# Kernel tuning notes

Hardware: AMD Instinct MI355X
Metric: run time of the kernel (lower is better)

## Reference

```python
import jax, jax.numpy as jnp
import numpy as np

B, N, F_IN, F_OUT, H = 8, 1024, 128, 64, 4
EPS = 1e-7
NEG_SLOPE = 0.2


def setup_inputs() -> dict:
    key = jax.random.key(0)
    k_a, k_x, k_w, k_aw, k_ab = jax.random.split(key, 5)
    A = jax.random.randint(k_a, (B, N, N), 0, 2).astype(jnp.float32)
    x = jax.random.normal(k_x, (B, N, F_IN), dtype=jnp.float32)
    # per-head params (stacked over head axis): GAT.W (xavier-normal-ish), attention Linear(2F->1)
    W = jax.random.normal(k_w, (H, F_IN, F_OUT), dtype=jnp.float32) * np.sqrt(2.0 / (F_IN + F_OUT))
    lim = 1.0 / np.sqrt(2 * F_OUT)
    a_w = jax.random.uniform(k_aw, (H, 2 * F_OUT), minval=-lim, maxval=lim, dtype=jnp.float32)
    a_b = jax.random.uniform(k_ab, (H,), minval=-lim, maxval=lim, dtype=jnp.float32)
    return {"A": A, "x": x, "W": W, "a_w": a_w, "a_b": a_b}


def reference(A, x, W, a_w, a_b):
    # Wh: (B, H, N, F_OUT)
    Wh = jnp.einsum('bnf,hfo->bhno', x, W)
    # attention linear on concat([Wh_i, Wh_j]) is separable: a1.Wh_i + a2.Wh_j + b
    a1, a2 = a_w[:, :F_OUT], a_w[:, F_OUT:]
    s_i = jnp.einsum('bhno,ho->bhn', Wh, a1)   # depends on row index i (dim 1 of (B,N,N))
    s_j = jnp.einsum('bhno,ho->bhn', Wh, a2)   # depends on col index j (dim 2)
    e = s_i[:, :, :, None] + s_j[:, :, None, :] + a_b[None, :, None, None]  # (B,H,Ni,Nj)
    e = jnp.where(e >= 0, e, NEG_SLOPE * e)  # LeakyReLU(0.2)
    # masked softmax as in source: exp, mask by A, normalize over dim=1 of (B,N,N) -> axis 2 here
    exps = jnp.exp(e) * A[:, None, :, :]
    attn = exps / (jnp.sum(exps, axis=2, keepdims=True) + EPS)
    out = jnp.einsum('bhij,bhjo->bhio', attn, Wh)  # matmul over j
    # concat heads on feature dim: (B, N, H*F_OUT)
    return out.transpose(0, 2, 1, 3).reshape(B, N, H * F_OUT)
```

## Files before the change

kernel.cpp:

```cpp
#include <hip/hip_runtime.h>
#include <hip/hip_bf16.h>
#include <hip/hip_fp16.h>

#define BB 8
#define NN 1024
#define FIN 128
#define FOUT 64
#define HH 4
#define EPSV 1e-7f
#define SLOPE 0.2f
#define LOG2E 1.44269504088896340736f

typedef _Float16 v8h __attribute__((ext_vector_type(8)));
typedef _Float16 v4h __attribute__((ext_vector_type(4)));
typedef _Float16 v2h __attribute__((ext_vector_type(2)));
typedef __fp16 v2hf __attribute__((ext_vector_type(2)));
typedef float v4f __attribute__((ext_vector_type(4)));

union U8 { v2h p[4]; v8h v; };
union U2 { v2hf hf; v2h h; };

__device__ __forceinline__ v2h clamp01(v2h x) {
  v2h zero = {(_Float16)0.0f, (_Float16)0.0f};
  v2h one = {(_Float16)1.0f, (_Float16)1.0f};
  return __builtin_elementwise_min(__builtin_elementwise_max(x, zero), one);
}

__device__ __forceinline__ v2h cvt2(float a, float b) {
  U2 u;
  u.hf = __builtin_amdgcn_cvt_pkrtz(a, b);
  return u.h;
}

__device__ __forceinline__ float dot2(v2h a, v2h b, float c) {
  U2 ua, ub;
  ua.h = a;
  ub.h = b;
  return __builtin_amdgcn_fdot2(ua.hf, ub.hf, c, false);
}

__global__ __launch_bounds__(256) void k0_wt(const float* __restrict__ W,
                                             _Float16* __restrict__ Wtt) {
  for (int it = 0; it < 16; ++it) {
    int idx = blockIdx.x * 4096 + it * 256 + threadIdx.x;
    int e = idx & 7, ln = (idx >> 3) & 15, kgg = (idx >> 7) & 15,
        ct = idx >> 11;
    int c = ct * 16 + ln, k = kgg * 8 + e;
    Wtt[idx] = (_Float16)W[(size_t)(c >> 6) * 8192 + k * 64 + (c & 63)];
  }
}

__global__ __launch_bounds__(256) void k1_whm(
    const float* __restrict__ x, const _Float16* __restrict__ Wtt,
    const float* __restrict__ aw, const float* __restrict__ ab,
    _Float16* __restrict__ WhH, float* __restrict__ si2,
    float* __restrict__ tj2, _Float16* __restrict__ tjh,
    _Float16* __restrict__ djh, _Float16* __restrict__ e2jh,
    float* __restrict__ e2i_t, float* __restrict__ di_t) {
  __shared__ _Float16 xs[16][136];
  int tid = threadIdx.x;
#pragma unroll
  for (int t2 = 0; t2 < 2; ++t2) {
    int idx = t2 * 256 + tid;
    int row = idx >> 5, c4 = (idx & 31) * 4;
    float4 v = *(const float4*)(x + ((size_t)blockIdx.x * 16 + row) * FIN + c4);
    v4h hv;
    hv[0] = (_Float16)v.x; hv[1] = (_Float16)v.y;
    hv[2] = (_Float16)v.z; hv[3] = (_Float16)v.w;
    *(v4h*)(&xs[row][c4]) = hv;
  }
  __syncthreads();
  int w = tid >> 6, l = tid & 63;
  int kg = l >> 4, ln = l & 15;
  v4f acc[4] = {{}, {}, {}, {}};
#pragma unroll
  for (int ks = 0; ks < 4; ++ks) {
    v8h af = *(const v8h*)(&xs[ln][ks * 32 + kg * 8]);
    int kgg = ks * 4 + kg;
#pragma unroll
    for (int t = 0; t < 4; ++t) {
      int ct = w * 4 + t;
      v8h bf = *(const v8h*)(Wtt + (((size_t)ct * 16 + kgg) * 16 + ln) * 8);
      acc[t] = __builtin_amdgcn_mfma_f32_16x16x32_f16(af, bf, acc[t], 0, 0, 0);
    }
  }
  float a1v[4], a2v[4];
#pragma unroll
  for (int t = 0; t < 4; ++t) {
    a1v[t] = aw[w * 128 + t * 16 + ln];
    a2v[t] = aw[w * 128 + 64 + t * 16 + ln];
  }
  float abv = ab[w];
#pragma unroll
  for (int r = 0; r < 4; ++r) {
    float v1 = acc[0][r] * a1v[0] + acc[1][r] * a1v[1] +
               acc[2][r] * a1v[2] + acc[3][r] * a1v[3];
    float v2 = acc[0][r] * a2v[0] + acc[1][r] * a2v[1] +
               acc[2][r] * a2v[2] + acc[3][r] * a2v[3];
#pragma unroll
    for (int off = 1; off < 16; off <<= 1) {
      v1 += __shfl_xor(v1, off);
      v2 += __shfl_xor(v2, off);
    }
    if (ln == 0) {
      int gr = blockIdx.x * 16 + kg * 4 + r;
      int b_ = gr >> 10, n_ = gr & 1023;
      size_t row = ((size_t)b_ * HH + w) * NN + n_;
      float v1L = v1 * LOG2E;
      float tjL = (v2 + abv) * LOG2E;
      si2[row] = v1L;
      tj2[row] = tjL;
      float e1i = __builtin_amdgcn_exp2f(v1L);
      float e2i = __builtin_amdgcn_exp2f(0.2f * v1L);
      e2i_t[row] = e2i;
      di_t[row] = e1i - e2i;
      float e1j = __builtin_amdgcn_exp2f(tjL);
      float e2j = __builtin_amdgcn_exp2f(0.2f * tjL);
      tjh[row] = (_Float16)tjL;
      e2jh[row] = (_Float16)e2j;
      djh[row] = (_Float16)(e1j - e2j);
    }
  }
#pragma unroll
  for (int t = 0; t < 4; ++t) {
#pragma unroll
    for (int r = 0; r < 4; ++r) {
      int gr = blockIdx.x * 16 + kg * 4 + r;
      int b_ = gr >> 10, n_ = gr & 1023;
      WhH[(((size_t)b_ * HH + w) * NN + n_) * 64 + (t * 16 + ln)] =
          (_Float16)acc[t][r];
    }
  }
}

__global__ __launch_bounds__(256) void kb_colsum_bits(
    const float* __restrict__ A, const float* __restrict__ si2,
    const float* __restrict__ e2i_t, const float* __restrict__ di_t,
    const _Float16* __restrict__ tjh, const _Float16* __restrict__ djh,
    const _Float16* __restrict__ e2jh, float* __restrict__ part,
    unsigned long long* __restrict__ Abits) {
  __shared__ v2h si_p[4][16], di_p[4][16], e2i_p[4][16];
  int b = blockIdx.z, is = blockIdx.y, jt = blockIdx.x;
  int tid = threadIdx.x;
  int w = tid >> 6, lane = tid & 63;
  int j = jt * 256 + tid;
  int i0 = is * 32;
  if (tid < 64) {
    int h = tid >> 4, pp = tid & 15;
    size_t row = ((size_t)(b * HH + h)) * NN + i0 + 2 * pp;
    si_p[h][pp] = cvt2(si2[row], si2[row + 1]);
    di_p[h][pp] = cvt2(di_t[row], di_t[row + 1]);
    e2i_p[h][pp] = cvt2(e2i_t[row], e2i_t[row + 1]);
  }
  __syncthreads();
  v2h tjb[4], djb[4], ejb[4];
#pragma unroll
  for (int h = 0; h < 4; ++h) {
    size_t jr = ((size_t)(b * HH + h)) * NN + j;
    _Float16 t = tjh[jr], d = djh[jr], e = e2jh[jr];
    tjb[h][0] = t; tjb[h][1] = t;
    djb[h][0] = d; djb[h][1] = d;
    ejb[h][0] = e; ejb[h][1] = e;
  }
  v2h big = {(_Float16)4096.0f, (_Float16)4096.0f};
  float acc[4] = {0.f, 0.f, 0.f, 0.f};
  const float* Ap = A + ((size_t)b * NN + i0) * NN + j;
  unsigned long long myword = 0ull;
#pragma unroll
  for (int c = 0; c < 4; ++c) {
    float av[8];
#pragma unroll
    for (int q = 0; q < 8; ++q) av[q] = Ap[(size_t)(c * 8 + q) * NN];
    v2h apk[4];
#pragma unroll
    for (int q = 0; q < 4; ++q) apk[q] = cvt2(av[2 * q], av[2 * q + 1]);
#pragma unroll
    for (int q = 0; q < 8; ++q) {
      unsigned long long m = __ballot(av[q] != 0.0f);
      if (lane == c * 8 + q) myword = m;
    }
#pragma unroll
    for (int h = 0; h < 4; ++h) {
      U8 si4, di4, ei4;
      si4.v = *(const v8h*)&si_p[h][c * 4];
      di4.v = *(const v8h*)&di_p[h][c * 4];
      ei4.v = *(const v8h*)&e2i_p[h][c * 4];
#pragma unroll
      for (int pp = 0; pp < 4; ++pp) {
        v2h f = si4.p[pp] + tjb[h];
        v2h s = clamp01(f * big);
        v2h ei = s * di4.p[pp] + ei4.p[pp];
        v2h ej = s * djb[h] + ejb[h];
        v2h p = ei * ej;
        acc[h] = dot2(p, apk[pp], acc[h]);
      }
    }
  }
  if (lane < 32)
    Abits[((size_t)b * NN + i0 + lane) * 16 + jt * 4 + w] = myword;
#pragma unroll
  for (int h = 0; h < 4; ++h)
    part[((size_t)(is * 32) + b * HH + h) * NN + j] = acc[h];
}

__global__ __launch_bounds__(256) void k3_scale_tr(
    const _Float16* __restrict__ WhH, const float* __restrict__ part,
    _Float16* __restrict__ VTt) {
  __shared__ float rbuf[64];
  __shared__ _Float16 tile[64 * 66];
  int bid = blockIdx.x;
  int b = bid & 7, rest = bid >> 3;
  int h = rest & 3, jt = rest >> 2;
  int bh = b * HH + h, j0 = jt * 64;
  int tid = threadIdx.x;
  if (tid < 64) {
    float s = 0.f;
#pragma unroll
    for (int is = 0; is < 32; ++is)
      s += part[((size_t)(is * 32) + bh) * NN + j0 + tid];
    rbuf[tid] = 1.0f / (s + EPSV);
  }
  __syncthreads();
#pragma unroll
  for (int it = 0; it < 16; ++it) {
    int lin = it * 256 + tid;
    int jj = lin >> 6, o = lin & 63;
    float v = (float)WhH[((size_t)bh * NN + j0 + jj) * 64 + o] * rbuf[jj];
    tile[o * 66 + jj] = (_Float16)v;
  }
  __syncthreads();
#pragma unroll
  for (int it = 0; it < 16; ++it) {
    int lin = it * 256 + tid;
    int o = lin >> 6, jj64 = lin & 63;
    int j = j0 + jj64;
    int jb = j >> 5, jj = j & 31;
    VTt[(((size_t)bh * 32 + jb) * 64 + o) * 32 + jj] = tile[o * 66 + jj64];
  }
}

__global__ __launch_bounds__(512, 4) void k4_pv(
    const unsigned long long* __restrict__ Abits,
    const float* __restrict__ si2, const _Float16* __restrict__ tjh,
    const _Float16* __restrict__ djh, const _Float16* __restrict__ e2jh,
    const float* __restrict__ e2i_t, const float* __restrict__ di_t,
    const _Float16* __restrict__ VTt, float* __restrict__ out) {
  __shared__ unsigned long long Ab[32][17];
  __shared__ _Float16 tjl[2][1024];
  __shared__ _Float16 djl[2][1024];
  __shared__ _Float16 e2jl[2][1024];
  __shared__ _Float16 lut[256][8];
  __shared__ float sil[2][32], e2il[2][32], dil[2][32];
  __shared__ float red[2][2][64][33];
  int bid = blockIdx.x;
  int b = bid & 7, hp = (bid >> 3) & 1, it = bid >> 4;
  int i0 = it * 32;
  int tid = threadIdx.x;
  {
    size_t base = (size_t)(b * HH + hp * 2) * NN;
    const unsigned int* s1 = (const unsigned int*)(tjh + base);
    const unsigned int* s2 = (const unsigned int*)(djh + base);
    const unsigned int* s3 = (const unsigned int*)(e2jh + base);
    unsigned int* d1 = (unsigned int*)&tjl[0][0];
    unsigned int* d2 = (unsigned int*)&djl[0][0];
    unsigned int* d3 = (unsigned int*)&e2jl[0][0];
    d1[tid] = s1[tid]; d1[tid + 512] = s1[tid + 512];
    d2[tid] = s2[tid]; d2[tid + 512] = s2[tid + 512];
    d3[tid] = s3[tid]; d3[tid + 512] = s3[tid + 512];
  }
  if (tid < 64) {
    int hh = tid >> 5, ii = tid & 31;
    size_t row = (size_t)(b * HH + hp * 2 + hh) * NN + i0 + ii;
    sil[hh][ii] = si2[row];
    e2il[hh][ii] = e2i_t[row];
    dil[hh][ii] = di_t[row];
  }
  if (tid < 256) {
#pragma unroll
    for (int e = 0; e < 8; ++e)
      lut[tid][e] = ((tid >> e) & 1) ? (_Float16)1.0f : (_Float16)0.0f;
  }
  {
    int row = tid >> 4, word = tid & 15;
    Ab[row][word] = Abits[((size_t)b * NN + i0 + row) * 16 + word];
  }
  __syncthreads();

  int w = tid >> 6, l = tid & 63;
  int hh = w & 1, jq4 = w >> 1;
  int kg = l >> 4, ln = l & 15;
  _Float16 sih0 = (_Float16)sil[hh][ln];
  _Float16 sih1 = (_Float16)sil[hh][16 + ln];
  v2h si0 = {sih0, sih0}, si1 = {sih1, sih1};
  _Float16 e2h0 = (_Float16)e2il[hh][ln], e2h1 = (_Float16)e2il[hh][16 + ln];
  _Float16 dih0 = (_Float16)dil[hh][ln], dih1 = (_Float16)dil[hh][16 + ln];
  v2h e2i0 = {e2h0, e2h0}, e2i1 = {e2h1, e2h1};
  v2h di0 = {dih0, dih0}, di1 = {dih1, dih1};
  v2h big = {(_Float16)4096.0f, (_Float16)4096.0f};
  int bh = b * HH + hp * 2 + hh;
  v4f acc0[4] = {{}, {}, {}, {}};
  v4f acc1[4] = {{}, {}, {}, {}};
  const _Float16* VTb = VTt + (size_t)bh * 32 * 64 * 32;
  int jbase = jq4 * 256;

#pragma unroll 2
  for (int jq = 0; jq < 8; ++jq) {
    int j = jbase + jq * 32 + kg * 8;
    int widx = j >> 6, sh = j & 63;
    unsigned int bits0 = (unsigned int)(Ab[ln][widx] >> sh) & 0xffu;
    unsigned int bits1 = (unsigned int)(Ab[16 + ln][widx] >> sh) & 0xffu;
    U8 tj8, dj8, ej8, m0, m1, af0, af1;
    tj8.v = *(const v8h*)&tjl[hh][j];
    dj8.v = *(const v8h*)&djl[hh][j];
    ej8.v = *(const v8h*)&e2jl[hh][j];
    m0.v = *(const v8h*)&lut[bits0][0];
    m1.v = *(const v8h*)&lut[bits1][0];
#pragma unroll
    for (int q = 0; q < 4; ++q) {
      v2h f0 = tj8.p[q] + si0;
      v2h s0 = clamp01(f0 * big);
      v2h ej0 = s0 * dj8.p[q] + ej8.p[q];
      v2h ei0 = s0 * di0 + e2i0;
      af0.p[q] = ei0 * ej0 * m0.p[q];
      v2h f1 = tj8.p[q] + si1;
      v2h s1v = clamp01(f1 * big);
      v2h ej1 = s1v * dj8.p[q] + ej8.p[q];
      v2h ei1 = s1v * di1 + e2i1;
      af1.p[q] = ei1 * ej1 * m1.p[q];
    }
    const _Float16* vb = VTb + (size_t)(j >> 5) * 2048 + kg * 8;
    v8h b0 = *(const v8h*)(vb + (0 * 16 + ln) * 32);
    v8h b1 = *(const v8h*)(vb + (1 * 16 + ln) * 32);
    v8h b2 = *(const v8h*)(vb + (2 * 16 + ln) * 32);
    v8h b3 = *(const v8h*)(vb + (3 * 16 + ln) * 32);
    acc0[0] = __builtin_amdgcn_mfma_f32_16x16x32_f16(af0.v, b0, acc0[0], 0, 0, 0);
    acc1[0] = __builtin_amdgcn_mfma_f32_16x16x32_f16(af1.v, b0, acc1[0], 0, 0, 0);
    acc0[1] = __builtin_amdgcn_mfma_f32_16x16x32_f16(af0.v, b1, acc0[1], 0, 0, 0);
    acc1[1] = __builtin_amdgcn_mfma_f32_16x16x32_f16(af1.v, b1, acc1[1], 0, 0, 0);
    acc0[2] = __builtin_amdgcn_mfma_f32_16x16x32_f16(af0.v, b2, acc0[2], 0, 0, 0);
    acc1[2] = __builtin_amdgcn_mfma_f32_16x16x32_f16(af1.v, b2, acc1[2], 0, 0, 0);
    acc0[3] = __builtin_amdgcn_mfma_f32_16x16x32_f16(af0.v, b3, acc0[3], 0, 0, 0);
    acc1[3] = __builtin_amdgcn_mfma_f32_16x16x32_f16(af1.v, b3, acc1[3], 0, 0, 0);
  }

  if (jq4 == 1 || jq4 == 3) {
    int slot = jq4 >> 1;
#pragma unroll
    for (int t = 0; t < 4; ++t)
#pragma unroll
      for (int r = 0; r < 4; ++r) {
        red[hh][slot][l][t * 4 + r] = acc0[t][r];
        red[hh][slot][l][16 + t * 4 + r] = acc1[t][r];
      }
  }
  __syncthreads();
  if (jq4 == 0 || jq4 == 2) {
    int slot = jq4 >> 1;
#pragma unroll
    for (int t = 0; t < 4; ++t)
#pragma unroll
      for (int r = 0; r < 4; ++r) {
        acc0[t][r] += red[hh][slot][l][t * 4 + r];
        acc1[t][r] += red[hh][slot][l][16 + t * 4 + r];
      }
  }
  __syncthreads();
  if (jq4 == 2) {
#pragma unroll
    for (int t = 0; t < 4; ++t)
#pragma unroll
      for (int r = 0; r < 4; ++r) {
        red[hh][0][l][t * 4 + r] = acc0[t][r];
        red[hh][0][l][16 + t * 4 + r] = acc1[t][r];
      }
  }
  __syncthreads();
  if (jq4 == 0) {
#pragma unroll
    for (int t = 0; t < 4; ++t)
#pragma unroll
      for (int r = 0; r < 4; ++r) {
        acc0[t][r] += red[hh][0][l][t * 4 + r];
        acc1[t][r] += red[hh][0][l][16 + t * 4 + r];
      }
#pragma unroll
    for (int r = 0; r < 4; ++r) {
      int gi0 = i0 + kg * 4 + r;
      float* op0 = out + ((size_t)b * NN + gi0) * 256 + (hp * 2 + hh) * 64;
      op0[0 * 16 + ln] = acc0[0][r];
      op0[1 * 16 + ln] = acc0[1][r];
      op0[2 * 16 + ln] = acc0[2][r];
      op0[3 * 16 + ln] = acc0[3][r];
      float* op1 = op0 + 16 * 256;
      op1[0 * 16 + ln] = acc1[0][r];
      op1[1 * 16 + ln] = acc1[1][r];
      op1[2 * 16 + ln] = acc1[2][r];
      op1[3 * 16 + ln] = acc1[3][r];
    }
  }
}

extern "C" void kernel_launch(void* const* d_in, const int* in_sizes, int n_in,
                              void* d_out, int out_size, void* d_ws,
                              size_t ws_size, hipStream_t stream) {
  const float* A = (const float*)d_in[0];
  const float* x = (const float*)d_in[1];
  const float* W = (const float*)d_in[2];
  const float* aw = (const float*)d_in[3];
  const float* ab = (const float*)d_in[4];
  float* out = (float*)d_out;
  char* ws = (char*)d_ws;
  _Float16* WhH = (_Float16*)ws;
  _Float16* VTt = (_Float16*)(ws + (4u << 20));
  _Float16* Wtt = (_Float16*)(ws + (8u << 20));
  float* si2 = (float*)(ws + (8u << 20) + (256u << 10));
  float* tj2 = (float*)(ws + (8u << 20) + (384u << 10));
  float* part = (float*)(ws + (8u << 20) + (512u << 10));
  unsigned long long* Abits =
      (unsigned long long*)(ws + (12u << 20) + (512u << 10));
  char* tb = ws + (13u << 20) + (512u << 10);
  _Float16* tjh = (_Float16*)tb;
  _Float16* djh = (_Float16*)(tb + (64u << 10));
  _Float16* e2jh = (_Float16*)(tb + (128u << 10));
  float* e2i_t = (float*)(tb + (192u << 10));
  float* di_t = (float*)(tb + (320u << 10));

  hipLaunchKernelGGL(k0_wt, dim3(8), dim3(256), 0, stream, W, Wtt);
  hipLaunchKernelGGL(k1_whm, dim3(512), dim3(256), 0, stream, x, Wtt, aw, ab,
                     WhH, si2, tj2, tjh, djh, e2jh, e2i_t, di_t);
  hipLaunchKernelGGL(kb_colsum_bits, dim3(4, 32, BB), dim3(256), 0, stream, A,
                     si2, e2i_t, di_t, tjh, djh, e2jh, part, Abits);
  hipLaunchKernelGGL(k3_scale_tr, dim3(512), dim3(256), 0, stream, WhH, part,
                     VTt);
  hipLaunchKernelGGL(k4_pv, dim3(512), dim3(512), 0, stream, Abits, si2, tjh,
                     djh, e2jh, e2i_t, di_t, VTt, out);
}
```

Baseline: 45.17 us.

## Fuse five kernel launches into one cooperative persistent kernel with grid syncs

Replaces the five-kernel pipeline (weight transpose, Wh matmul, column-sum/bitmask, scale-transpose, PV) with one cooperative kernel of 256 blocks of 512 threads. The stages are separated by grid.sync, and each block loops over two work units per stage. The aim is to remove per-launch overhead and the gaps between kernels. The cost is grid-wide barriers, a fixed grid size that may leave some CUs idle, and more register and LDS pressure from the shared union. The old multi-kernel path is kept as a fallback if the cooperative launch fails, and the unused tj2 buffer is dropped.

```diff
diff --git a/kernel.cpp b/kernel.cpp
--- a/kernel.cpp
+++ b/kernel.cpp
@@ -1,6 +1,9 @@
 #include <hip/hip_runtime.h>
 #include <hip/hip_bf16.h>
 #include <hip/hip_fp16.h>
+#include <hip/hip_cooperative_groups.h>
+
+namespace cg = cooperative_groups;
 
 #define BB 8
 #define NN 1024
@@ -39,6 +42,389 @@
   return __builtin_amdgcn_fdot2(ua.hf, ub.hf, c, false);
 }
 
+struct SK1 { _Float16 xs[16][136]; };
+struct SKB { v2h si_p[2][4][16], di_p[2][4][16], e2i_p[2][4][16]; };
+struct SK3 { float rbuf[64]; _Float16 tile[64 * 66]; };
+struct SK4 {
+  unsigned long long Ab[32][17];
+  _Float16 tjl[2][1024], djl[2][1024], e2jl[2][1024];
+  _Float16 lut[256][8];
+  float sil[2][32], e2il[2][32], dil[2][32];
+  float red[2][2][64][33];
+};
+union Smem { SK1 k1; SKB kb; SK3 k3; SK4 k4; };
+
+__global__ __launch_bounds__(512, 2) void mega(
+    const float* __restrict__ A, const float* __restrict__ x,
+    const float* __restrict__ W, const float* __restrict__ aw,
+    const float* __restrict__ ab, _Float16* __restrict__ WhH,
+    _Float16* __restrict__ VTt, _Float16* __restrict__ Wtt,
+    float* __restrict__ si2, float* __restrict__ part,
+    unsigned long long* __restrict__ Abits, _Float16* __restrict__ tjh,
+    _Float16* __restrict__ djh, _Float16* __restrict__ e2jh,
+    float* __restrict__ e2i_t, float* __restrict__ di_t,
+    float* __restrict__ out) {
+  __shared__ Smem sm;
+  cg::grid_group grid = cg::this_grid();
+  int bid = blockIdx.x;
+  int tid = threadIdx.x;
+
+  if (bid < 8) {
+#pragma unroll
+    for (int it = 0; it < 8; ++it) {
+      int idx = bid * 4096 + it * 512 + tid;
+      int e = idx & 7, ln = (idx >> 3) & 15, kgg = (idx >> 7) & 15,
+          ct = idx >> 11;
+      int c = ct * 16 + ln, k = kgg * 8 + e;
+      Wtt[idx] = (_Float16)W[(size_t)(c >> 6) * 8192 + k * 64 + (c & 63)];
+    }
+  }
+  grid.sync();
+
+  for (int r = 0; r < 2; ++r) {
+    int tile = bid + r * 256;
+    if (r) __syncthreads();
+    {
+      int row = tid >> 5, c4 = (tid & 31) * 4;
+      float4 v = *(const float4*)(x + ((size_t)tile * 16 + row) * FIN + c4);
+      v4h hv;
+      hv[0] = (_Float16)v.x; hv[1] = (_Float16)v.y;
+      hv[2] = (_Float16)v.z; hv[3] = (_Float16)v.w;
+      *(v4h*)(&sm.k1.xs[row][c4]) = hv;
+    }
+    __syncthreads();
+    if (tid < 256) {
+      int w = tid >> 6, l = tid & 63;
+      int kg = l >> 4, ln = l & 15;
+      v4f acc[4] = {{}, {}, {}, {}};
+#pragma unroll
+      for (int ks = 0; ks < 4; ++ks) {
+        v8h af = *(const v8h*)(&sm.k1.xs[ln][ks * 32 + kg * 8]);
+        int kgg = ks * 4 + kg;
+#pragma unroll
+        for (int t = 0; t < 4; ++t) {
+          int ct = w * 4 + t;
+          v8h bf =
+              *(const v8h*)(Wtt + (((size_t)ct * 16 + kgg) * 16 + ln) * 8);
+          acc[t] =
+              __builtin_amdgcn_mfma_f32_16x16x32_f16(af, bf, acc[t], 0, 0, 0);
+        }
+      }
+      float a1v[4], a2v[4];
+#pragma unroll
+      for (int t = 0; t < 4; ++t) {
+        a1v[t] = aw[w * 128 + t * 16 + ln];
+        a2v[t] = aw[w * 128 + 64 + t * 16 + ln];
+      }
+      float abv = ab[w];
+#pragma unroll
+      for (int rr2 = 0; rr2 < 4; ++rr2) {
+        float v1 = acc[0][rr2] * a1v[0] + acc[1][rr2] * a1v[1] +
+                   acc[2][rr2] * a1v[2] + acc[3][rr2] * a1v[3];
+        float v2 = acc[0][rr2] * a2v[0] + acc[1][rr2] * a2v[1] +
+                   acc[2][rr2] * a2v[2] + acc[3][rr2] * a2v[3];
+#pragma unroll
+        for (int off = 1; off < 16; off <<= 1) {
+          v1 += __shfl_xor(v1, off);
+          v2 += __shfl_xor(v2, off);
+        }
+        if (ln == 0) {
+          int gr = tile * 16 + kg * 4 + rr2;
+          int b_ = gr >> 10, n_ = gr & 1023;
+          size_t rw = ((size_t)b_ * HH + w) * NN + n_;
+          float v1L = v1 * LOG2E;
+          float tjL = (v2 + abv) * LOG2E;
+          si2[rw] = v1L;
+          float e1i = __builtin_amdgcn_exp2f(v1L);
+          float e2i = __builtin_amdgcn_exp2f(0.2f * v1L);
+          e2i_t[rw] = e2i;
+          di_t[rw] = e1i - e2i;
+          float e1j = __builtin_amdgcn_exp2f(tjL);
+          float e2j = __builtin_amdgcn_exp2f(0.2f * tjL);
+          tjh[rw] = (_Float16)tjL;
+          e2jh[rw] = (_Float16)e2j;
+          djh[rw] = (_Float16)(e1j - e2j);
+        }
+      }
+#pragma unroll
+      for (int t = 0; t < 4; ++t) {
+#pragma unroll
+        for (int rr2 = 0; rr2 < 4; ++rr2) {
+          int gr = tile * 16 + kg * 4 + rr2;
+          int b_ = gr >> 10, n_ = gr & 1023;
+          WhH[(((size_t)b_ * HH + w) * NN + n_) * 64 + (t * 16 + ln)] =
+              (_Float16)acc[t][rr2];
+        }
+      }
+    }
+  }
+  grid.sync();
+
+  for (int r = 0; r < 2; ++r) {
+    int unit = tid >> 8, lt = tid & 255;
+    int u = r * 512 + bid * 2 + unit;
+    int jt = u & 3, is = (u >> 2) & 31, b = u >> 7;
+    int w = lt >> 6, lane = lt & 63;
+    int j = jt * 256 + lt;
+    int i0 = is * 32;
+    if (r) __syncthreads();
+    if (lt < 64) {
+      int h = lt >> 4, pp = lt & 15;
+      size_t row = ((size_t)(b * HH + h)) * NN + i0 + 2 * pp;
+      sm.kb.si_p[unit][h][pp] = cvt2(si2[row], si2[row + 1]);
+      sm.kb.di_p[unit][h][pp] = cvt2(di_t[row], di_t[row + 1]);
+      sm.kb.e2i_p[unit][h][pp] = cvt2(e2i_t[row], e2i_t[row + 1]);
+    }
+    __syncthreads();
+    v2h tjb[4], djb[4], ejb[4];
+#pragma unroll
+    for (int h = 0; h < 4; ++h) {
+      size_t jr = ((size_t)(b * HH + h)) * NN + j;
+      _Float16 t = tjh[jr], d = djh[jr], e = e2jh[jr];
+      tjb[h][0] = t; tjb[h][1] = t;
+      djb[h][0] = d; djb[h][1] = d;
+      ejb[h][0] = e; ejb[h][1] = e;
+    }
+    v2h big = {(_Float16)4096.0f, (_Float16)4096.0f};
+    float acc[4] = {0.f, 0.f, 0.f, 0.f};
+    const float* Ap = A + ((size_t)b * NN + i0) * NN + j;
+    unsigned long long myword = 0ull;
+#pragma unroll
+    for (int c = 0; c < 4; ++c) {
+      float av[8];
+#pragma unroll
+      for (int q = 0; q < 8; ++q) av[q] = Ap[(size_t)(c * 8 + q) * NN];
+      v2h apk[4];
+#pragma unroll
+      for (int q = 0; q < 4; ++q) apk[q] = cvt2(av[2 * q], av[2 * q + 1]);
+#pragma unroll
+      for (int q = 0; q < 8; ++q) {
+        unsigned long long m = __ballot(av[q] != 0.0f);
+        if (lane == c * 8 + q) myword = m;
+      }
+#pragma unroll
+      for (int h = 0; h < 4; ++h) {
+        U8 si4, di4, ei4;
+        si4.v = *(const v8h*)&sm.kb.si_p[unit][h][c * 4];
+        di4.v = *(const v8h*)&sm.kb.di_p[unit][h][c * 4];
+        ei4.v = *(const v8h*)&sm.kb.e2i_p[unit][h][c * 4];
+#pragma unroll
+        for (int pp = 0; pp < 4; ++pp) {
+          v2h f = si4.p[pp] + tjb[h];
+          v2h s = clamp01(f * big);
+          v2h ei = s * di4.p[pp] + ei4.p[pp];
+          v2h ej = s * djb[h] + ejb[h];
+          v2h p = ei * ej;
+          acc[h] = dot2(p, apk[pp], acc[h]);
+        }
+      }
+    }
+    if (lane < 32)
+      Abits[((size_t)b * NN + i0 + lane) * 16 + jt * 4 + w] = myword;
+#pragma unroll
+    for (int h = 0; h < 4; ++h)
+      part[((size_t)(is * 32) + b * HH + h) * NN + j] = acc[h];
+  }
+  grid.sync();
+
+  for (int r = 0; r < 2; ++r) {
+    int bid9 = bid + r * 256;
+    int b = bid9 & 7, rest = bid9 >> 3;
+    int h = rest & 3, jt = rest >> 2;
+    int bh = b * HH + h, j0 = jt * 64;
+    if (r) __syncthreads();
+    if (tid < 64) {
+      float s = 0.f;
+#pragma unroll
+      for (int is = 0; is < 32; ++is)
+        s += part[((size_t)(is * 32) + bh) * NN + j0 + tid];
+      sm.k3.rbuf[tid] = 1.0f / (s + EPSV);
+    }
+    __syncthreads();
+#pragma unroll
+    for (int it = 0; it < 8; ++it) {
+      int lin = it * 512 + tid;
+      int jj = lin >> 6, o = lin & 63;
+      float v =
+          (float)WhH[((size_t)bh * NN + j0 + jj) * 64 + o] * sm.k3.rbuf[jj];
+      sm.k3.tile[o * 66 + jj] = (_Float16)v;
+    }
+    __syncthreads();
+#pragma unroll
+    for (int it = 0; it < 8; ++it) {
+      int lin = it * 512 + tid;
+      int o = lin >> 6, jj64 = lin & 63;
+      int j = j0 + jj64;
+      int jb = j >> 5, jj = j & 31;
+      VTt[(((size_t)bh * 32 + jb) * 64 + o) * 32 + jj] =
+          sm.k3.tile[o * 66 + jj64];
+    }
+  }
+  grid.sync();
+
+  {
+    int b = bid & 7, hp = (bid >> 3) & 1;
+    {
+      size_t base = (size_t)(b * HH + hp * 2) * NN;
+      const unsigned int* s1 = (const unsigned int*)(tjh + base);
+      const unsigned int* s2 = (const unsigned int*)(djh + base);
+      const unsigned int* s3 = (const unsigned int*)(e2jh + base);
+      unsigned int* d1 = (unsigned int*)&sm.k4.tjl[0][0];
+      unsigned int* d2 = (unsigned int*)&sm.k4.djl[0][0];
+      unsigned int* d3 = (unsigned int*)&sm.k4.e2jl[0][0];
+      d1[tid] = s1[tid]; d1[tid + 512] = s1[tid + 512];
+      d2[tid] = s2[tid]; d2[tid + 512] = s2[tid + 512];
+      d3[tid] = s3[tid]; d3[tid + 512] = s3[tid + 512];
+    }
+    if (tid < 256) {
+#pragma unroll
+      for (int e = 0; e < 8; ++e)
+        sm.k4.lut[tid][e] = ((tid >> e) & 1) ? (_Float16)1.0f : (_Float16)0.0f;
+    }
+    for (int r = 0; r < 2; ++r) {
+      int it = (bid >> 4) + r * 16;
+      int i0 = it * 32;
+      if (tid < 64) {
+        int hh = tid >> 5, ii = tid & 31;
+        size_t row = (size_t)(b * HH + hp * 2 + hh) * NN + i0 + ii;
+        sm.k4.sil[hh][ii] = si2[row];
+        sm.k4.e2il[hh][ii] = e2i_t[row];
+        sm.k4.dil[hh][ii] = di_t[row];
+      }
+      {
+        int row = tid >> 4, word = tid & 15;
+        sm.k4.Ab[row][word] = Abits[((size_t)b * NN + i0 + row) * 16 + word];
+      }
+      __syncthreads();
+
+      int w = tid >> 6, l = tid & 63;
+      int hh = w & 1, jq4 = w >> 1;
+      int kg = l >> 4, ln = l & 15;
+      _Float16 sih0 = (_Float16)sm.k4.sil[hh][ln];
+      _Float16 sih1 = (_Float16)sm.k4.sil[hh][16 + ln];
+      v2h si0 = {sih0, sih0}, si1 = {sih1, sih1};
+      _Float16 e2h0 = (_Float16)sm.k4.e2il[hh][ln],
+               e2h1 = (_Float16)sm.k4.e2il[hh][16 + ln];
+      _Float16 dih0 = (_Float16)sm.k4.dil[hh][ln],
+               dih1 = (_Float16)sm.k4.dil[hh][16 + ln];
+      v2h e2i0 = {e2h0, e2h0}, e2i1 = {e2h1, e2h1};
+      v2h di0 = {dih0, dih0}, di1 = {dih1, dih1};
+      v2h big = {(_Float16)4096.0f, (_Float16)4096.0f};
+      int bh = b * HH + hp * 2 + hh;
+      v4f acc0[4] = {{}, {}, {}, {}};
+      v4f acc1[4] = {{}, {}, {}, {}};
+      const _Float16* VTb = VTt + (size_t)bh * 32 * 64 * 32;
+      int jbase = jq4 * 256;
+
+#pragma unroll 2
+      for (int jq = 0; jq < 8; ++jq) {
+        int j = jbase + jq * 32 + kg * 8;
+        int widx = j >> 6, sh = j & 63;
+        unsigned int bits0 = (unsigned int)(sm.k4.Ab[ln][widx] >> sh) & 0xffu;
+        unsigned int bits1 =
+            (unsigned int)(sm.k4.Ab[16 + ln][widx] >> sh) & 0xffu;
+        U8 tj8, dj8, ej8, m0, m1, af0, af1;
+        tj8.v = *(const v8h*)&sm.k4.tjl[hh][j];
+        dj8.v = *(const v8h*)&sm.k4.djl[hh][j];
+        ej8.v = *(const v8h*)&sm.k4.e2jl[hh][j];
+        m0.v = *(const v8h*)&sm.k4.lut[bits0][0];
+        m1.v = *(const v8h*)&sm.k4.lut[bits1][0];
+#pragma unroll
+        for (int q = 0; q < 4; ++q) {
+          v2h f0 = tj8.p[q] + si0;
+          v2h s0 = clamp01(f0 * big);
+          v2h ej0 = s0 * dj8.p[q] + ej8.p[q];
+          v2h ei0 = s0 * di0 + e2i0;
+          af0.p[q] = ei0 * ej0 * m0.p[q];
+          v2h f1 = tj8.p[q] + si1;
+          v2h s1v = clamp01(f1 * big);
+          v2h ej1 = s1v * dj8.p[q] + ej8.p[q];
+          v2h ei1 = s1v * di1 + e2i1;
+          af1.p[q] = ei1 * ej1 * m1.p[q];
+        }
+        const _Float16* vb = VTb + (size_t)(j >> 5) * 2048 + kg * 8;
+        v8h b0 = *(const v8h*)(vb + (0 * 16 + ln) * 32);
+        v8h b1 = *(const v8h*)(vb + (1 * 16 + ln) * 32);
+        v8h b2 = *(const v8h*)(vb + (2 * 16 + ln) * 32);
+        v8h b3 = *(const v8h*)(vb + (3 * 16 + ln) * 32);
+        acc0[0] = __builtin_amdgcn_mfma_f32_16x16x32_f16(af0.v, b0, acc0[0],
+                                                         0, 0, 0);
+        acc1[0] = __builtin_amdgcn_mfma_f32_16x16x32_f16(af1.v, b0, acc1[0],
+                                                         0, 0, 0);
+        acc0[1] = __builtin_amdgcn_mfma_f32_16x16x32_f16(af0.v, b1, acc0[1],
+                                                         0, 0, 0);
+        acc1[1] = __builtin_amdgcn_mfma_f32_16x16x32_f16(af1.v, b1, acc1[1],
+                                                         0, 0, 0);
+        acc0[2] = __builtin_amdgcn_mfma_f32_16x16x32_f16(af0.v, b2, acc0[2],
+                                                         0, 0, 0);
+        acc1[2] = __builtin_amdgcn_mfma_f32_16x16x32_f16(af1.v, b2, acc1[2],
+                                                         0, 0, 0);
+        acc0[3] = __builtin_amdgcn_mfma_f32_16x16x32_f16(af0.v, b3, acc0[3],
+                                                         0, 0, 0);
+        acc1[3] = __builtin_amdgcn_mfma_f32_16x16x32_f16(af1.v, b3, acc1[3],
+                                                         0, 0, 0);
+      }
+
+      if (jq4 == 1 || jq4 == 3) {
+        int slot = jq4 >> 1;
+#pragma unroll
+        for (int t = 0; t < 4; ++t)
+#pragma unroll
+          for (int rr2 = 0; rr2 < 4; ++rr2) {
+            sm.k4.red[hh][slot][l][t * 4 + rr2] = acc0[t][rr2];
+            sm.k4.red[hh][slot][l][16 + t * 4 + rr2] = acc1[t][rr2];
+          }
+      }
+      __syncthreads();
+      if (jq4 == 0 || jq4 == 2) {
+        int slot = jq4 >> 1;
+#pragma unroll
+        for (int t = 0; t < 4; ++t)
+#pragma unroll
+          for (int rr2 = 0; rr2 < 4; ++rr2) {
+            acc0[t][rr2] += sm.k4.red[hh][slot][l][t * 4 + rr2];
+            acc1[t][rr2] += sm.k4.red[hh][slot][l][16 + t * 4 + rr2];
+          }
+      }
+      __syncthreads();
+      if (jq4 == 2) {
+#pragma unroll
+        for (int t = 0; t < 4; ++t)
+#pragma unroll
+          for (int rr2 = 0; rr2 < 4; ++rr2) {
+            sm.k4.red[hh][0][l][t * 4 + rr2] = acc0[t][rr2];
+            sm.k4.red[hh][0][l][16 + t * 4 + rr2] = acc1[t][rr2];
+          }
+      }
+      __syncthreads();
+      if (jq4 == 0) {
+#pragma unroll
+        for (int t = 0; t < 4; ++t)
+#pragma unroll
+          for (int rr2 = 0; rr2 < 4; ++rr2) {
+            acc0[t][rr2] += sm.k4.red[hh][0][l][t * 4 + rr2];
+            acc1[t][rr2] += sm.k4.red[hh][0][l][16 + t * 4 + rr2];
+          }
+#pragma unroll
+        for (int rr2 = 0; rr2 < 4; ++rr2) {
+          int gi0 = i0 + kg * 4 + rr2;
+          float* op0 = out + ((size_t)b * NN + gi0) * 256 + (hp * 2 + hh) * 64;
+          op0[0 * 16 + ln] = acc0[0][rr2];
+          op0[1 * 16 + ln] = acc0[1][rr2];
+          op0[2 * 16 + ln] = acc0[2][rr2];
+          op0[3 * 16 + ln] = acc0[3][rr2];
+          float* op1 = op0 + 16 * 256;
+          op1[0 * 16 + ln] = acc1[0][rr2];
+          op1[1 * 16 + ln] = acc1[1][rr2];
+          op1[2 * 16 + ln] = acc1[2][rr2];
+          op1[3 * 16 + ln] = acc1[3][rr2];
+        }
+      }
+      __syncthreads();
+    }
+  }
+}
+
 __global__ __launch_bounds__(256) void k0_wt(const float* __restrict__ W,
                                              _Float16* __restrict__ Wtt) {
   for (int it = 0; it < 16; ++it) {
@@ -54,9 +440,9 @@
     const float* __restrict__ x, const _Float16* __restrict__ Wtt,
     const float* __restrict__ aw, const float* __restrict__ ab,
     _Float16* __restrict__ WhH, float* __restrict__ si2,
-    float* __restrict__ tj2, _Float16* __restrict__ tjh,
-    _Float16* __restrict__ djh, _Float16* __restrict__ e2jh,
-    float* __restrict__ e2i_t, float* __restrict__ di_t) {
+    _Float16* __restrict__ tjh, _Float16* __restrict__ djh,
+    _Float16* __restrict__ e2jh, float* __restrict__ e2i_t,
+    float* __restrict__ di_t) {
   __shared__ _Float16 xs[16][136];
   int tid = threadIdx.x;
 #pragma unroll
@@ -109,7 +495,6 @@
       float v1L = v1 * LOG2E;
       float tjL = (v2 + abv) * LOG2E;
       si2[row] = v1L;
-      tj2[row] = tjL;
       float e1i = __builtin_amdgcn_exp2f(v1L);
       float e2i = __builtin_amdgcn_exp2f(0.2f * v1L);
       e2i_t[row] = e2i;
@@ -414,7 +799,6 @@
   _Float16* VTt = (_Float16*)(ws + (4u << 20));
   _Float16* Wtt = (_Float16*)(ws + (8u << 20));
   float* si2 = (float*)(ws + (8u << 20) + (256u << 10));
-  float* tj2 = (float*)(ws + (8u << 20) + (384u << 10));
   float* part = (float*)(ws + (8u << 20) + (512u << 10));
   unsigned long long* Abits =
       (unsigned long long*)(ws + (12u << 20) + (512u << 10));
@@ -425,13 +809,22 @@
   float* e2i_t = (float*)(tb + (192u << 10));
   float* di_t = (float*)(tb + (320u << 10));
 
-  hipLaunchKernelGGL(k0_wt, dim3(8), dim3(256), 0, stream, W, Wtt);
-  hipLaunchKernelGGL(k1_whm, dim3(512), dim3(256), 0, stream, x, Wtt, aw, ab,
-                     WhH, si2, tj2, tjh, djh, e2jh, e2i_t, di_t);
-  hipLaunchKernelGGL(kb_colsum_bits, dim3(4, 32, BB), dim3(256), 0, stream, A,
-                     si2, e2i_t, di_t, tjh, djh, e2jh, part, Abits);
-  hipLaunchKernelGGL(k3_scale_tr, dim3(512), dim3(256), 0, stream, WhH, part,
-                     VTt);
-  hipLaunchKernelGGL(k4_pv, dim3(512), dim3(512), 0, stream, Abits, si2, tjh,
-                     djh, e2jh, e2i_t, di_t, VTt, out);
-}
+  void* args[] = {(void*)&A,     (void*)&x,    (void*)&W,     (void*)&aw,
+                  (void*)&ab,    (void*)&WhH,  (void*)&VTt,   (void*)&Wtt,
+                  (void*)&si2,   (void*)&part, (void*)&Abits, (void*)&tjh,
+                  (void*)&djh,   (void*)&e2jh, (void*)&e2i_t, (void*)&di_t,
+                  (void*)&out};
+  hipError_t err = hipLaunchCooperativeKernel((void*)mega, dim3(256),
+                                              dim3(512), args, 0, stream);
+  if (err != hipSuccess) {
+    hipLaunchKernelGGL(k0_wt, dim3(8), dim3(256), 0, stream, W, Wtt);
+    hipLaunchKernelGGL(k1_whm, dim3(512), dim3(256), 0, stream, x, Wtt, aw,
+                       ab, WhH, si2, tjh, djh, e2jh, e2i_t, di_t);
+    hipLaunchKernelGGL(kb_colsum_bits, dim3(4, 32, BB), dim3(256), 0, stream,
+                       A, si2, e2i_t, di_t, tjh, djh, e2jh, part, Abits);
+    hipLaunchKernelGGL(k3_scale_tr, dim3(512), dim3(256), 0, stream, WhH,
+                       part, VTt);
+    hipLaunchKernelGGL(k4_pv, dim3(512), dim3(512), 0, stream, Abits, si2,
+                       tjh, djh, e2jh, e2i_t, di_t, VTt, out);
+  }
+}
```

After: 174.0 us. +285.3%, slower.

## Double k4 row tile to 64 rows per block to reuse V fragments

Applied to the files above, without the earlier changes.

The PV kernel now handles 64 query rows per block instead of 32, so each loaded V fragment and per-column tj/dj/e2j vector feeds four MFMA row fragments instead of two. The grid is halved to 256 blocks and the cross-wave reduction runs in two passes over fragment pairs. This cuts repeated VTt and LDS staging traffic per output but raises accumulator register pressure (64 floats per lane) and halves the block count, which may lower occupancy on a 256-CU part. The unused tj2 write in k1 is also removed.

```diff
diff --git a/kernel.cpp b/kernel.cpp
--- a/kernel.cpp
+++ b/kernel.cpp
@@ -54,9 +54,9 @@
     const float* __restrict__ x, const _Float16* __restrict__ Wtt,
     const float* __restrict__ aw, const float* __restrict__ ab,
     _Float16* __restrict__ WhH, float* __restrict__ si2,
-    float* __restrict__ tj2, _Float16* __restrict__ tjh,
-    _Float16* __restrict__ djh, _Float16* __restrict__ e2jh,
-    float* __restrict__ e2i_t, float* __restrict__ di_t) {
+    _Float16* __restrict__ tjh, _Float16* __restrict__ djh,
+    _Float16* __restrict__ e2jh, float* __restrict__ e2i_t,
+    float* __restrict__ di_t) {
   __shared__ _Float16 xs[16][136];
   int tid = threadIdx.x;
 #pragma unroll
@@ -109,7 +109,6 @@
       float v1L = v1 * LOG2E;
       float tjL = (v2 + abv) * LOG2E;
       si2[row] = v1L;
-      tj2[row] = tjL;
       float e1i = __builtin_amdgcn_exp2f(v1L);
       float e2i = __builtin_amdgcn_exp2f(0.2f * v1L);
       e2i_t[row] = e2i;
@@ -245,16 +244,16 @@
     const _Float16* __restrict__ djh, const _Float16* __restrict__ e2jh,
     const float* __restrict__ e2i_t, const float* __restrict__ di_t,
     const _Float16* __restrict__ VTt, float* __restrict__ out) {
-  __shared__ unsigned long long Ab[32][17];
+  __shared__ unsigned long long Ab[64][17];
   __shared__ _Float16 tjl[2][1024];
   __shared__ _Float16 djl[2][1024];
   __shared__ _Float16 e2jl[2][1024];
   __shared__ _Float16 lut[256][8];
-  __shared__ float sil[2][32], e2il[2][32], dil[2][32];
+  __shared__ float sil[2][64], e2il[2][64], dil[2][64];
   __shared__ float red[2][2][64][33];
   int bid = blockIdx.x;
   int b = bid & 7, hp = (bid >> 3) & 1, it = bid >> 4;
-  int i0 = it * 32;
+  int i0 = it * 64;
   int tid = threadIdx.x;
   {
     size_t base = (size_t)(b * HH + hp * 2) * NN;
@@ -268,8 +267,8 @@
     d2[tid] = s2[tid]; d2[tid + 512] = s2[tid + 512];
     d3[tid] = s3[tid]; d3[tid + 512] = s3[tid + 512];
   }
-  if (tid < 64) {
-    int hh = tid >> 5, ii = tid & 31;
+  if (tid < 128) {
+    int hh = tid >> 6, ii = tid & 63;
     size_t row = (size_t)(b * HH + hp * 2 + hh) * NN + i0 + ii;
     sil[hh][ii] = si2[row];
     e2il[hh][ii] = e2i_t[row];
@@ -281,121 +280,128 @@
       lut[tid][e] = ((tid >> e) & 1) ? (_Float16)1.0f : (_Float16)0.0f;
   }
   {
-    int row = tid >> 4, word = tid & 15;
-    Ab[row][word] = Abits[((size_t)b * NN + i0 + row) * 16 + word];
+#pragma unroll
+    for (int t2 = 0; t2 < 2; ++t2) {
+      int idx = t2 * 512 + tid;
+      int row = idx >> 4, word = idx & 15;
+      Ab[row][word] = Abits[((size_t)b * NN + i0 + row) * 16 + word];
+    }
   }
   __syncthreads();
 
   int w = tid >> 6, l = tid & 63;
   int hh = w & 1, jq4 = w >> 1;
   int kg = l >> 4, ln = l & 15;
-  _Float16 sih0 = (_Float16)sil[hh][ln];
-  _Float16 sih1 = (_Float16)sil[hh][16 + ln];
-  v2h si0 = {sih0, sih0}, si1 = {sih1, sih1};
-  _Float16 e2h0 = (_Float16)e2il[hh][ln], e2h1 = (_Float16)e2il[hh][16 + ln];
-  _Float16 dih0 = (_Float16)dil[hh][ln], dih1 = (_Float16)dil[hh][16 + ln];
-  v2h e2i0 = {e2h0, e2h0}, e2i1 = {e2h1, e2h1};
-  v2h di0 = {dih0, dih0}, di1 = {dih1, dih1};
+  v2h si_f[4], e2_f[4], di_f[4];
+#pragma unroll
+  for (int f = 0; f < 4; ++f) {
+    _Float16 s = (_Float16)sil[hh][f * 16 + ln];
+    _Float16 e = (_Float16)e2il[hh][f * 16 + ln];
+    _Float16 d = (_Float16)dil[hh][f * 16 + ln];
+    si_f[f][0] = s; si_f[f][1] = s;
+    e2_f[f][0] = e; e2_f[f][1] = e;
+    di_f[f][0] = d; di_f[f][1] = d;
+  }
   v2h big = {(_Float16)4096.0f, (_Float16)4096.0f};
   int bh = b * HH + hp * 2 + hh;
-  v4f acc0[4] = {{}, {}, {}, {}};
-  v4f acc1[4] = {{}, {}, {}, {}};
+  v4f acc[4][4] = {};
   const _Float16* VTb = VTt + (size_t)bh * 32 * 64 * 32;
   int jbase = jq4 * 256;
 
-#pragma unroll 2
   for (int jq = 0; jq < 8; ++jq) {
     int j = jbase + jq * 32 + kg * 8;
     int widx = j >> 6, sh = j & 63;
-    unsigned int bits0 = (unsigned int)(Ab[ln][widx] >> sh) & 0xffu;
-    unsigned int bits1 = (unsigned int)(Ab[16 + ln][widx] >> sh) & 0xffu;
-    U8 tj8, dj8, ej8, m0, m1, af0, af1;
+    U8 tj8, dj8, ej8;
     tj8.v = *(const v8h*)&tjl[hh][j];
     dj8.v = *(const v8h*)&djl[hh][j];
     ej8.v = *(const v8h*)&e2jl[hh][j];
-    m0.v = *(const v8h*)&lut[bits0][0];
-    m1.v = *(const v8h*)&lut[bits1][0];
-#pragma unroll
-    for (int q = 0; q < 4; ++q) {
-      v2h f0 = tj8.p[q] + si0;
-      v2h s0 = clamp01(f0 * big);
-      v2h ej0 = s0 * dj8.p[q] + ej8.p[q];
-      v2h ei0 = s0 * di0 + e2i0;
-      af0.p[q] = ei0 * ej0 * m0.p[q];
-      v2h f1 = tj8.p[q] + si1;
-      v2h s1v = clamp01(f1 * big);
-      v2h ej1 = s1v * dj8.p[q] + ej8.p[q];
-      v2h ei1 = s1v * di1 + e2i1;
-      af1.p[q] = ei1 * ej1 * m1.p[q];
-    }
     const _Float16* vb = VTb + (size_t)(j >> 5) * 2048 + kg * 8;
     v8h b0 = *(const v8h*)(vb + (0 * 16 + ln) * 32);
     v8h b1 = *(const v8h*)(vb + (1 * 16 + ln) * 32);
     v8h b2 = *(const v8h*)(vb + (2 * 16 + ln) * 32);
     v8h b3 = *(const v8h*)(vb + (3 * 16 + ln) * 32);
-    acc0[0] = __builtin_amdgcn_mfma_f32_16x16x32_f16(af0.v, b0, acc0[0], 0, 0, 0);
-    acc1[0] = __builtin_amdgcn_mfma_f32_16x16x32_f16(af1.v, b0, acc1[0], 0, 0, 0);
-    acc0[1] = __builtin_amdgcn_mfma_f32_16x16x32_f16(af0.v, b1, acc0[1], 0, 0, 0);
-    acc1[1] = __builtin_amdgcn_mfma_f32_16x16x32_f16(af1.v, b1, acc1[1], 0, 0, 0);
-    acc0[2] = __builtin_amdgcn_mfma_f32_16x16x32_f16(af0.v, b2, acc0[2], 0, 0, 0);
-    acc1[2] = __builtin_amdgcn_mfma_f32_16x16x32_f16(af1.v, b2, acc1[2], 0, 0, 0);
-    acc0[3] = __builtin_amdgcn_mfma_f32_16x16x32_f16(af0.v, b3, acc0[3], 0, 0, 0);
-    acc1[3] = __builtin_amdgcn_mfma_f32_16x16x32_f16(af1.v, b3, acc1[3], 0, 0, 0);
-  }
-
-  if (jq4 == 1 || jq4 == 3) {
-    int slot = jq4 >> 1;
-#pragma unroll
-    for (int t = 0; t < 4; ++t)
+#pragma unroll
+    for (int f = 0; f < 4; ++f) {
+      unsigned int bits = (unsigned int)(Ab[f * 16 + ln][widx] >> sh) & 0xffu;
+      U8 m, af;
+      m.v = *(const v8h*)&lut[bits][0];
+#pragma unroll
+      for (int q = 0; q < 4; ++q) {
+        v2h fv = tj8.p[q] + si_f[f];
+        v2h s = clamp01(fv * big);
+        v2h ej = s * dj8.p[q] + ej8.p[q];
+        v2h ei = s * di_f[f] + e2_f[f];
+        af.p[q] = ei * ej * m.p[q];
+      }
+      acc[f][0] =
+          __builtin_amdgcn_mfma_f32_16x16x32_f16(af.v, b0, acc[f][0], 0, 0, 0);
+      acc[f][1] =
+          __builtin_amdgcn_mfma_f32_16x16x32_f16(af.v, b1, acc[f][1], 0, 0, 0);
+      acc[f][2] =
+          __builtin_amdgcn_mfma_f32_16x16x32_f16(af.v, b2, acc[f][2], 0, 0, 0);
+      acc[f][3] =
+          __builtin_amdgcn_mfma_f32_16x16x32_f16(af.v, b3, acc[f][3], 0, 0, 0);
+    }
+  }
+
+#pragma unroll
+  for (int pass = 0; pass < 2; ++pass) {
+    int fA = pass * 2, fB = pass * 2 + 1;
+    if (pass) __syncthreads();
+    if (jq4 == 1 || jq4 == 3) {
+      int slot = jq4 >> 1;
+#pragma unroll
+      for (int t = 0; t < 4; ++t)
+#pragma unroll
+        for (int r = 0; r < 4; ++r) {
+          red[hh][slot][l][t * 4 + r] = acc[fA][t][r];
+          red[hh][slot][l][16 + t * 4 + r] = acc[fB][t][r];
+        }
+    }
+    __syncthreads();
+    if (jq4 == 0 || jq4 == 2) {
+      int slot = jq4 >> 1;
+#pragma unroll
+      for (int t = 0; t < 4; ++t)
+#pragma unroll
+        for (int r = 0; r < 4; ++r) {
+          acc[fA][t][r] += red[hh][slot][l][t * 4 + r];
+          acc[fB][t][r] += red[hh][slot][l][16 + t * 4 + r];
+        }
+    }
+    __syncthreads();
+    if (jq4 == 2) {
+#pragma unroll
+      for (int t = 0; t < 4; ++t)
+#pragma unroll
+        for (int r = 0; r < 4; ++r) {
+          red[hh][0][l][t * 4 + r] = acc[fA][t][r];
+          red[hh][0][l][16 + t * 4 + r] = acc[fB][t][r];
+        }
+    }
+    __syncthreads();
+    if (jq4 == 0) {
+#pragma unroll
+      for (int t = 0; t < 4; ++t)
+#pragma unroll
+        for (int r = 0; r < 4; ++r) {
+          acc[fA][t][r] += red[hh][0][l][t * 4 + r];
+          acc[fB][t][r] += red[hh][0][l][16 + t * 4 + r];
+        }
 #pragma unroll
       for (int r = 0; r < 4; ++r) {
-        red[hh][slot][l][t * 4 + r] = acc0[t][r];
-        red[hh][slot][l][16 + t * 4 + r] = acc1[t][r];
+        int giA = i0 + fA * 16 + kg * 4 + r;
+        float* opA = out + ((size_t)b * NN + giA) * 256 + (hp * 2 + hh) * 64;
+        opA[0 * 16 + ln] = acc[fA][0][r];
+        opA[1 * 16 + ln] = acc[fA][1][r];
+        opA[2 * 16 + ln] = acc[fA][2][r];
+        opA[3 * 16 + ln] = acc[fA][3][r];
+        float* opB = opA + 16 * 256;
+        opB[0 * 16 + ln] = acc[fB][0][r];
+        opB[1 * 16 + ln] = acc[fB][1][r];
+        opB[2 * 16 + ln] = acc[fB][2][r];
+        opB[3 * 16 + ln] = acc[fB][3][r];
       }
-  }
-  __syncthreads();
-  if (jq4 == 0 || jq4 == 2) {
-    int slot = jq4 >> 1;
-#pragma unroll
-    for (int t = 0; t < 4; ++t)
-#pragma unroll
-      for (int r = 0; r < 4; ++r) {
-        acc0[t][r] += red[hh][slot][l][t * 4 + r];
-        acc1[t][r] += red[hh][slot][l][16 + t * 4 + r];
-      }
-  }
-  __syncthreads();
-  if (jq4 == 2) {
-#pragma unroll
-    for (int t = 0; t < 4; ++t)
-#pragma unroll
-      for (int r = 0; r < 4; ++r) {
-        red[hh][0][l][t * 4 + r] = acc0[t][r];
-        red[hh][0][l][16 + t * 4 + r] = acc1[t][r];
-      }
-  }
-  __syncthreads();
-  if (jq4 == 0) {
-#pragma unroll
-    for (int t = 0; t < 4; ++t)
-#pragma unroll
-      for (int r = 0; r < 4; ++r) {
-        acc0[t][r] += red[hh][0][l][t * 4 + r];
-        acc1[t][r] += red[hh][0][l][16 + t * 4 + r];
-      }
-#pragma unroll
-    for (int r = 0; r < 4; ++r) {
-      int gi0 = i0 + kg * 4 + r;
-      float* op0 = out + ((size_t)b * NN + gi0) * 256 + (hp * 2 + hh) * 64;
-      op0[0 * 16 + ln] = acc0[0][r];
-      op0[1 * 16 + ln] = acc0[1][r];
-      op0[2 * 16 + ln] = acc0[2][r];
-      op0[3 * 16 + ln] = acc0[3][r];
-      float* op1 = op0 + 16 * 256;
-      op1[0 * 16 + ln] = acc1[0][r];
-      op1[1 * 16 + ln] = acc1[1][r];
-      op1[2 * 16 + ln] = acc1[2][r];
-      op1[3 * 16 + ln] = acc1[3][r];
     }
   }
 }
@@ -414,7 +420,6 @@
   _Float16* VTt = (_Float16*)(ws + (4u << 20));
   _Float16* Wtt = (_Float16*)(ws + (8u << 20));
   float* si2 = (float*)(ws + (8u << 20) + (256u << 10));
-  float* tj2 = (float*)(ws + (8u << 20) + (384u << 10));
   float* part = (float*)(ws + (8u << 20) + (512u << 10));
   unsigned long long* Abits =
       (unsigned long long*)(ws + (12u << 20) + (512u << 10));
@@ -427,11 +432,11 @@
 
   hipLaunchKernelGGL(k0_wt, dim3(8), dim3(256), 0, stream, W, Wtt);
   hipLaunchKernelGGL(k1_whm, dim3(512), dim3(256), 0, stream, x, Wtt, aw, ab,
-                     WhH, si2, tj2, tjh, djh, e2jh, e2i_t, di_t);
+                     WhH, si2, tjh, djh, e2jh, e2i_t, di_t);
   hipLaunchKernelGGL(kb_colsum_bits, dim3(4, 32, BB), dim3(256), 0, stream, A,
                      si2, e2i_t, di_t, tjh, djh, e2jh, part, Abits);
   hipLaunchKernelGGL(k3_scale_tr, dim3(512), dim3(256), 0, stream, WhH, part,
                      VTt);
-  hipLaunchKernelGGL(k4_pv, dim3(512), dim3(512), 0, stream, Abits, si2, tjh,
+  hipLaunchKernelGGL(k4_pv, dim3(256), dim3(512), 0, stream, Abits, si2, tjh,
                      djh, e2jh, e2i_t, di_t, VTt, out);
 }
```

Result: no change. 44.73 us (-1.0%).
